# Kernel tuning notes

Hardware: AMD Instinct MI355X
Metric: run time of the kernel (lower is better)

Reference implementation:

```python
import jax, jax.numpy as jnp
import numpy as np

B, T, I, H = 64, 1024, 256, 256


def setup_inputs() -> dict:
    key = jax.random.key(0)
    ks = jax.random.split(key, 7)
    s_in = 1.0 / np.sqrt(I)
    s_h = 1.0 / np.sqrt(H)
    return {
        "x": jax.random.normal(ks[0], (B, T, I), dtype=jnp.float32),
        "W_ih0": jax.random.normal(ks[1], (H, I), dtype=jnp.float32) * s_in,
        "b_ih0": jax.random.normal(ks[2], (H,), dtype=jnp.float32) * s_in,
        "W_hh0": jax.random.normal(ks[3], (H, H), dtype=jnp.float32) * s_h,
        "W_ih1": jax.random.normal(ks[4], (H, H), dtype=jnp.float32) * s_h,
        "b_ih1": jax.random.normal(ks[5], (H,), dtype=jnp.float32) * s_h,
        "W_hh1": jax.random.normal(ks[6], (H, H), dtype=jnp.float32) * s_h,
    }


def _elman_layer(x, W_ih, b_ih, W_hh):
    # Batch the input projection across all timesteps (the fusion the torch
    # loop misses), then scan only the sequential hidden update.
    xp = jnp.einsum("bti,hi->bth", x, W_ih) + b_ih  # [B,T,H]
    h0 = jnp.zeros((x.shape[0], W_hh.shape[0]), dtype=x.dtype)

    def step(h, xt):  # xt: [B,H]
        h = jnp.tanh(xt + h @ W_hh.T)
        return h, h

    _, ys = jax.lax.scan(step, h0, jnp.swapaxes(xp, 0, 1))  # [T,B,H]
    return jnp.swapaxes(ys, 0, 1)  # [B,T,H]


def reference(x, W_ih0, b_ih0, W_hh0, W_ih1, b_ih1, W_hh1):
    h = _elman_layer(x, W_ih0, b_ih0, W_hh0)
    h = _elman_layer(h, W_ih1, b_ih1, W_hh1)
    return h
```

## Files before the change

### kernel.cpp

```cpp
#include <hip/hip_runtime.h>
#include <cstdint>


#define HDIM 256
#define TLEN 1024
#define BATCH 64

__global__ __launch_bounds__(256) void proj_gemm(
    const float* __restrict__ X,
    const float* __restrict__ W,
    const float* __restrict__ bias,
    float* __restrict__ C, int M)
{
    __shared__ __align__(16) float Ast[16][136];
    __shared__ __align__(16) float Bst[16][68];

    const int tid = threadIdx.x;
    const int tx  = tid & 15;
    const int ty  = tid >> 4;
    const int m0  = blockIdx.x * 128;
    const int n0  = blockIdx.y * 64;

    float acc[8][4];
#pragma unroll
    for (int i = 0; i < 8; ++i)
#pragma unroll
        for (int j = 0; j < 4; ++j) acc[i][j] = 0.f;

    const int ar = tid >> 1;
    const int ah = (tid & 1) * 8;
    const int bn = tid >> 2;
    const int bg = (tid & 3) * 4;

    for (int kc = 0; kc < 16; ++kc) {
        const int k0 = kc * 16;
        const float4 av0 = *reinterpret_cast<const float4*>(&X[(size_t)(m0 + ar) * HDIM + k0 + ah]);
        const float4 av1 = *reinterpret_cast<const float4*>(&X[(size_t)(m0 + ar) * HDIM + k0 + ah + 4]);
        const float4 bv  = *reinterpret_cast<const float4*>(&W[(size_t)(n0 + bn) * HDIM + k0 + bg]);
        __syncthreads();
        Ast[ah + 0][ar] = av0.x; Ast[ah + 1][ar] = av0.y;
        Ast[ah + 2][ar] = av0.z; Ast[ah + 3][ar] = av0.w;
        Ast[ah + 4][ar] = av1.x; Ast[ah + 5][ar] = av1.y;
        Ast[ah + 6][ar] = av1.z; Ast[ah + 7][ar] = av1.w;
        Bst[bg + 0][bn] = bv.x;  Bst[bg + 1][bn] = bv.y;
        Bst[bg + 2][bn] = bv.z;  Bst[bg + 3][bn] = bv.w;
        __syncthreads();
#pragma unroll
        for (int kk = 0; kk < 16; ++kk) {
            const float4 a0 = *reinterpret_cast<const float4*>(&Ast[kk][ty * 8]);
            const float4 a1 = *reinterpret_cast<const float4*>(&Ast[kk][ty * 8 + 4]);
            const float4 b4 = *reinterpret_cast<const float4*>(&Bst[kk][tx * 4]);
            const float av[8] = {a0.x, a0.y, a0.z, a0.w, a1.x, a1.y, a1.z, a1.w};
            const float bb[4] = {b4.x, b4.y, b4.z, b4.w};
#pragma unroll
            for (int i = 0; i < 8; ++i)
#pragma unroll
                for (int j = 0; j < 4; ++j)
                    acc[i][j] = fmaf(av[i], bb[j], acc[i][j]);
        }
    }

    const float4 bias4 = *reinterpret_cast<const float4*>(&bias[n0 + tx * 4]);
    const float bb[4] = {bias4.x, bias4.y, bias4.z, bias4.w};
#pragma unroll
    for (int i = 0; i < 8; ++i) {
        float4 o;
        o.x = acc[i][0] + bb[0];
        o.y = acc[i][1] + bb[1];
        o.z = acc[i][2] + bb[2];
        o.w = acc[i][3] + bb[3];
        *reinterpret_cast<float4*>(&C[(size_t)(m0 + ty * 8 + i) * HDIM + n0 + tx * 4]) = o;
    }
}

__device__ __forceinline__ float fast_tanh(float x)
{
    const float xc = fminf(fmaxf(x, -15.f), 15.f);
    const float e  = __expf(2.f * xc);
    return (e - 1.f) / (e + 1.f);
}

__global__ __launch_bounds__(1024) void elman_scan(
    const float* __restrict__ xp,
    const float* __restrict__ Whh,
    float* __restrict__ y,
    int T)
{
    const int b   = blockIdx.x;
    const int tid = threadIdx.x;
    const int j   = tid & 255;
    const int q   = tid >> 8;

    float4 w[16];
    const float4* wp = reinterpret_cast<const float4*>(Whh + (size_t)j * HDIM + q * 64);
#pragma unroll
    for (int c = 0; c < 16; ++c) w[c] = wp[c];

    __shared__ __align__(16) float hs[HDIM];
    __shared__ float red[3][HDIM];
    __shared__ float xpb[2][HDIM];

    const float* xrow = xp + (size_t)b * T * HDIM;
    float*       yrow = y  + (size_t)b * T * HDIM;

    if (q == 0) {
        hs[j] = 0.f;
        xpb[0][j] = xrow[j];
    }
    __syncthreads();

    for (int t = 0; t < T; ++t) {
        const float4* h4 = reinterpret_cast<const float4*>(&hs[q * 64]);
        float s0 = 0.f, s1 = 0.f, s2 = 0.f, s3 = 0.f;
#pragma unroll
        for (int c = 0; c < 16; c += 4) {
            const float4 h0 = h4[c + 0];
            const float4 h1 = h4[c + 1];
            const float4 h2 = h4[c + 2];
            const float4 h3 = h4[c + 3];
            s0 = fmaf(w[c + 0].x, h0.x, s0); s0 = fmaf(w[c + 0].y, h0.y, s0);
            s0 = fmaf(w[c + 0].z, h0.z, s0); s0 = fmaf(w[c + 0].w, h0.w, s0);
            s1 = fmaf(w[c + 1].x, h1.x, s1); s1 = fmaf(w[c + 1].y, h1.y, s1);
            s1 = fmaf(w[c + 1].z, h1.z, s1); s1 = fmaf(w[c + 1].w, h1.w, s1);
            s2 = fmaf(w[c + 2].x, h2.x, s2); s2 = fmaf(w[c + 2].y, h2.y, s2);
            s2 = fmaf(w[c + 2].z, h2.z, s2); s2 = fmaf(w[c + 2].w, h2.w, s2);
            s3 = fmaf(w[c + 3].x, h3.x, s3); s3 = fmaf(w[c + 3].y, h3.y, s3);
            s3 = fmaf(w[c + 3].z, h3.z, s3); s3 = fmaf(w[c + 3].w, h3.w, s3);
        }
        const float s = (s0 + s1) + (s2 + s3);

        if (q) red[q - 1][j] = s;
        __syncthreads();

        if (q == 0) {
            const float tot = s + red[0][j] + red[1][j] + red[2][j] + xpb[t & 1][j];
            const float hn  = fast_tanh(tot);
            hs[j] = hn;
            yrow[(size_t)t * HDIM + j] = hn;
        } else if (q == 1) {
            if (t + 1 < T) xpb[(t + 1) & 1][j] = xrow[(size_t)(t + 1) * HDIM + j];
        }
        __syncthreads();
    }
}

extern "C" void kernel_launch(void* const* d_in, const int* in_sizes, int n_in,
                              void* d_out, int out_size, void* d_ws, size_t ws_size,
                              hipStream_t stream)
{
    const float* x     = (const float*)d_in[0];
    const float* W_ih0 = (const float*)d_in[1];
    const float* b_ih0 = (const float*)d_in[2];
    const float* W_hh0 = (const float*)d_in[3];
    const float* W_ih1 = (const float*)d_in[4];
    const float* b_ih1 = (const float*)d_in[5];
    const float* W_hh1 = (const float*)d_in[6];

    float* out = (float*)d_out;
    float* xp  = (float*)d_ws;

    const int M = BATCH * TLEN;
    dim3 ggrid(M / 128, HDIM / 64);

    proj_gemm<<<ggrid, 256, 0, stream>>>(x,   W_ih0, b_ih0, xp, M);
    elman_scan<<<BATCH, 1024, 0, stream>>>(xp, W_hh0, out, TLEN);
    proj_gemm<<<ggrid, 256, 0, stream>>>(out, W_ih1, b_ih1, xp, M);
    elman_scan<<<BATCH, 1024, 0, stream>>>(xp, W_hh1, out, TLEN);
}
```

Measured before the change: 2.026 ms.

## Split recurrent dot across lane pairs with shuffle reduce and one barrier per step

The scan kernel drops from 1024 to 512 threads. Each hidden unit is now computed by two adjacent lanes, each holding half the W_hh row (128 floats) in registers, and the partial sums are combined with a shuffle instead of a shared-memory reduction. The hidden state is double-buffered in shared memory so each timestep needs one barrier instead of two, and the xp values are prefetched two steps ahead into registers. The cost is doubled register pressure per thread, which risks spills or lower occupancy, and a longer serial FMA chain per step.

```diff
diff --git a/kernel.cpp b/kernel.cpp
--- a/kernel.cpp
+++ b/kernel.cpp
@@ -80,67 +80,76 @@
     return (e - 1.f) / (e + 1.f);
 }
 
-__global__ __launch_bounds__(1024) void elman_scan(
+__device__ __forceinline__ float dot128(const float4* __restrict__ w,
+                                        const float*  __restrict__ hb)
+{
+    const float4* h4 = reinterpret_cast<const float4*>(hb);
+    float s0 = 0.f, s1 = 0.f, s2 = 0.f, s3 = 0.f;
+#pragma unroll
+    for (int c = 0; c < 32; c += 4) {
+        const float4 h0 = h4[c + 0];
+        const float4 h1 = h4[c + 1];
+        const float4 h2 = h4[c + 2];
+        const float4 h3 = h4[c + 3];
+        s0 = fmaf(w[c + 0].x, h0.x, s0); s0 = fmaf(w[c + 0].y, h0.y, s0);
+        s0 = fmaf(w[c + 0].z, h0.z, s0); s0 = fmaf(w[c + 0].w, h0.w, s0);
+        s1 = fmaf(w[c + 1].x, h1.x, s1); s1 = fmaf(w[c + 1].y, h1.y, s1);
+        s1 = fmaf(w[c + 1].z, h1.z, s1); s1 = fmaf(w[c + 1].w, h1.w, s1);
+        s2 = fmaf(w[c + 2].x, h2.x, s2); s2 = fmaf(w[c + 2].y, h2.y, s2);
+        s2 = fmaf(w[c + 2].z, h2.z, s2); s2 = fmaf(w[c + 2].w, h2.w, s2);
+        s3 = fmaf(w[c + 3].x, h3.x, s3); s3 = fmaf(w[c + 3].y, h3.y, s3);
+        s3 = fmaf(w[c + 3].z, h3.z, s3); s3 = fmaf(w[c + 3].w, h3.w, s3);
+    }
+    return (s0 + s1) + (s2 + s3);
+}
+
+__global__ __launch_bounds__(512, 2) void elman_scan(
     const float* __restrict__ xp,
     const float* __restrict__ Whh,
     float* __restrict__ y,
     int T)
 {
-    const int b   = blockIdx.x;
-    const int tid = threadIdx.x;
-    const int j   = tid & 255;
-    const int q   = tid >> 8;
+    const int b    = blockIdx.x;
+    const int tid  = threadIdx.x;
+    const int j    = tid >> 1;
+    const int half = tid & 1;
 
-    float4 w[16];
-    const float4* wp = reinterpret_cast<const float4*>(Whh + (size_t)j * HDIM + q * 64);
+    float4 w[32];
+    const float4* wp = reinterpret_cast<const float4*>(Whh + (size_t)j * HDIM + half * 128);
 #pragma unroll
-    for (int c = 0; c < 16; ++c) w[c] = wp[c];
+    for (int c = 0; c < 32; ++c) w[c] = wp[c];
 
-    __shared__ __align__(16) float hs[HDIM];
-    __shared__ float red[3][HDIM];
-    __shared__ float xpb[2][HDIM];
+    __shared__ __align__(16) float hbuf[2][HDIM];
 
     const float* xrow = xp + (size_t)b * T * HDIM;
     float*       yrow = y  + (size_t)b * T * HDIM;
 
-    if (q == 0) {
-        hs[j] = 0.f;
-        xpb[0][j] = xrow[j];
-    }
+    if (half == 0) hbuf[0][j] = 0.f;
+    float x0 = xrow[j];
+    float x1 = xrow[HDIM + j];
     __syncthreads();
 
-    for (int t = 0; t < T; ++t) {
-        const float4* h4 = reinterpret_cast<const float4*>(&hs[q * 64]);
-        float s0 = 0.f, s1 = 0.f, s2 = 0.f, s3 = 0.f;
-#pragma unroll
-        for (int c = 0; c < 16; c += 4) {
-            const float4 h0 = h4[c + 0];
-            const float4 h1 = h4[c + 1];
-            const float4 h2 = h4[c + 2];
-            const float4 h3 = h4[c + 3];
-            s0 = fmaf(w[c + 0].x, h0.x, s0); s0 = fmaf(w[c + 0].y, h0.y, s0);
-            s0 = fmaf(w[c + 0].z, h0.z, s0); s0 = fmaf(w[c + 0].w, h0.w, s0);
-            s1 = fmaf(w[c + 1].x, h1.x, s1); s1 = fmaf(w[c + 1].y, h1.y, s1);
-            s1 = fmaf(w[c + 1].z, h1.z, s1); s1 = fmaf(w[c + 1].w, h1.w, s1);
-            s2 = fmaf(w[c + 2].x, h2.x, s2); s2 = fmaf(w[c + 2].y, h2.y, s2);
-            s2 = fmaf(w[c + 2].z, h2.z, s2); s2 = fmaf(w[c + 2].w, h2.w, s2);
-            s3 = fmaf(w[c + 3].x, h3.x, s3); s3 = fmaf(w[c + 3].y, h3.y, s3);
-            s3 = fmaf(w[c + 3].z, h3.z, s3); s3 = fmaf(w[c + 3].w, h3.w, s3);
+    for (int t = 0; t < T; t += 2) {
+        {
+            const float xnew = (t + 2 < T) ? xrow[(size_t)(t + 2) * HDIM + j] : 0.f;
+            float s = dot128(w, &hbuf[0][half * 128]);
+            s += __shfl_xor(s, 1);
+            const float hn = fast_tanh(s + x0);
+            if (half == 0) hbuf[1][j] = hn;
+            else           yrow[(size_t)t * HDIM + j] = hn;
+            x0 = xnew;
+            __syncthreads();
         }
-        const float s = (s0 + s1) + (s2 + s3);
-
-        if (q) red[q - 1][j] = s;
-        __syncthreads();
-
-        if (q == 0) {
-            const float tot = s + red[0][j] + red[1][j] + red[2][j] + xpb[t & 1][j];
-            const float hn  = fast_tanh(tot);
-            hs[j] = hn;
-            yrow[(size_t)t * HDIM + j] = hn;
-        } else if (q == 1) {
-            if (t + 1 < T) xpb[(t + 1) & 1][j] = xrow[(size_t)(t + 1) * HDIM + j];
+        {
+            const float xnew = (t + 3 < T) ? xrow[(size_t)(t + 3) * HDIM + j] : 0.f;
+            float s = dot128(w, &hbuf[1][half * 128]);
+            s += __shfl_xor(s, 1);
+            const float hn = fast_tanh(s + x1);
+            if (half == 0) hbuf[0][j] = hn;
+            else           yrow[(size_t)(t + 1) * HDIM + j] = hn;
+            x1 = xnew;
+            __syncthreads();
         }
-        __syncthreads();
     }
 }
 
@@ -163,7 +172,7 @@
     dim3 ggrid(M / 128, HDIM / 64);
 
     proj_gemm<<<ggrid, 256, 0, stream>>>(x,   W_ih0, b_ih0, xp, M);
-    elman_scan<<<BATCH, 1024, 0, stream>>>(xp, W_hh0, out, TLEN);
+    elman_scan<<<BATCH, 512, 0, stream>>>(xp, W_hh0, out, TLEN);
     proj_gemm<<<ggrid, 256, 0, stream>>>(out, W_ih1, b_ih1, xp, M);
-    elman_scan<<<BATCH, 1024, 0, stream>>>(xp, W_hh1, out, TLEN);
+    elman_scan<<<BATCH, 512, 0, stream>>>(xp, W_hh1, out, TLEN);
 }
```

Result: slower. 2.460 ms (+21.4%).

## Reduce scan partial sums with wave shuffles and double-buffer hidden state

Applied to the files above, without the earlier changes.

The scan kernel now places the four K-quarter partial dot products for each hidden unit in adjacent lanes of one wave and combines them with xor shuffles, instead of going through a shared-memory reduction array. The hidden state is double-buffered in padded LDS, which cuts the per-timestep barriers from two to one. Input projections are prefetched into registers four steps ahead through a rolling buffer. The aim is to shorten the serial per-timestep critical path of barriers and LDS round-trips. In exchange, every lane now computes the tanh redundantly, and the launch_bounds occupancy hint may add register pressure.

```diff
diff --git a/kernel.cpp b/kernel.cpp
--- a/kernel.cpp
+++ b/kernel.cpp
@@ -5,6 +5,7 @@
 #define HDIM 256
 #define TLEN 1024
 #define BATCH 64
+#define HQ 68
 
 __global__ __launch_bounds__(256) void proj_gemm(
     const float* __restrict__ X,
@@ -80,67 +81,78 @@
     return (e - 1.f) / (e + 1.f);
 }
 
-__global__ __launch_bounds__(1024) void elman_scan(
+__global__ __launch_bounds__(1024, 4) void elman_scan(
     const float* __restrict__ xp,
     const float* __restrict__ Whh,
     float* __restrict__ y,
     int T)
 {
-    const int b   = blockIdx.x;
-    const int tid = threadIdx.x;
-    const int j   = tid & 255;
-    const int q   = tid >> 8;
+    const int b    = blockIdx.x;
+    const int tid  = threadIdx.x;
+    const int lane = tid & 63;
+    const int wave = tid >> 6;
+    const int j    = wave * 16 + (lane >> 2);
+    const int q    = lane & 3;
 
     float4 w[16];
-    const float4* wp = reinterpret_cast<const float4*>(Whh + (size_t)j * HDIM + q * 64);
+    {
+        const float4* wp = reinterpret_cast<const float4*>(Whh + (size_t)j * HDIM + q * 64);
 #pragma unroll
-    for (int c = 0; c < 16; ++c) w[c] = wp[c];
+        for (int c = 0; c < 16; ++c) w[c] = wp[c];
+    }
 
-    __shared__ __align__(16) float hs[HDIM];
-    __shared__ float red[3][HDIM];
-    __shared__ float xpb[2][HDIM];
+    __shared__ __align__(16) float hbuf[2][4 * HQ];
 
     const float* xrow = xp + (size_t)b * T * HDIM;
     float*       yrow = y  + (size_t)b * T * HDIM;
 
-    if (q == 0) {
-        hs[j] = 0.f;
-        xpb[0][j] = xrow[j];
-    }
+    const int hpos = (j >> 6) * HQ + (j & 63);
+    if (q == 0) hbuf[0][hpos] = 0.f;
+
+    float xv[4];
+#pragma unroll
+    for (int p = 0; p < 4; ++p) xv[p] = xrow[(size_t)p * HDIM + j];
+
     __syncthreads();
 
-    for (int t = 0; t < T; ++t) {
-        const float4* h4 = reinterpret_cast<const float4*>(&hs[q * 64]);
-        float s0 = 0.f, s1 = 0.f, s2 = 0.f, s3 = 0.f;
+    int cur = 0;
+    for (int t = 0; t < T; t += 4) {
 #pragma unroll
-        for (int c = 0; c < 16; c += 4) {
-            const float4 h0 = h4[c + 0];
-            const float4 h1 = h4[c + 1];
-            const float4 h2 = h4[c + 2];
-            const float4 h3 = h4[c + 3];
-            s0 = fmaf(w[c + 0].x, h0.x, s0); s0 = fmaf(w[c + 0].y, h0.y, s0);
-            s0 = fmaf(w[c + 0].z, h0.z, s0); s0 = fmaf(w[c + 0].w, h0.w, s0);
-            s1 = fmaf(w[c + 1].x, h1.x, s1); s1 = fmaf(w[c + 1].y, h1.y, s1);
-            s1 = fmaf(w[c + 1].z, h1.z, s1); s1 = fmaf(w[c + 1].w, h1.w, s1);
-            s2 = fmaf(w[c + 2].x, h2.x, s2); s2 = fmaf(w[c + 2].y, h2.y, s2);
-            s2 = fmaf(w[c + 2].z, h2.z, s2); s2 = fmaf(w[c + 2].w, h2.w, s2);
-            s3 = fmaf(w[c + 3].x, h3.x, s3); s3 = fmaf(w[c + 3].y, h3.y, s3);
-            s3 = fmaf(w[c + 3].z, h3.z, s3); s3 = fmaf(w[c + 3].w, h3.w, s3);
+        for (int p = 0; p < 4; ++p) {
+            int tf = t + p + 4; tf = (tf < T) ? tf : (T - 1);
+            const float xnew = xrow[(size_t)tf * HDIM + j];
+
+            const float* hb = &hbuf[cur][q * HQ];
+            float s0 = 0.f, s1 = 0.f, s2 = 0.f, s3 = 0.f;
+#pragma unroll
+            for (int c = 0; c < 16; c += 4) {
+                const float4 h0 = *reinterpret_cast<const float4*>(hb + (c + 0) * 4);
+                const float4 h1 = *reinterpret_cast<const float4*>(hb + (c + 1) * 4);
+                const float4 h2 = *reinterpret_cast<const float4*>(hb + (c + 2) * 4);
+                const float4 h3 = *reinterpret_cast<const float4*>(hb + (c + 3) * 4);
+                s0 = fmaf(w[c + 0].x, h0.x, s0); s0 = fmaf(w[c + 0].y, h0.y, s0);
+                s0 = fmaf(w[c + 0].z, h0.z, s0); s0 = fmaf(w[c + 0].w, h0.w, s0);
+                s1 = fmaf(w[c + 1].x, h1.x, s1); s1 = fmaf(w[c + 1].y, h1.y, s1);
+                s1 = fmaf(w[c + 1].z, h1.z, s1); s1 = fmaf(w[c + 1].w, h1.w, s1);
+                s2 = fmaf(w[c + 2].x, h2.x, s2); s2 = fmaf(w[c + 2].y, h2.y, s2);
+                s2 = fmaf(w[c + 2].z, h2.z, s2); s2 = fmaf(w[c + 2].w, h2.w, s2);
+                s3 = fmaf(w[c + 3].x, h3.x, s3); s3 = fmaf(w[c + 3].y, h3.y, s3);
+                s3 = fmaf(w[c + 3].z, h3.z, s3); s3 = fmaf(w[c + 3].w, h3.w, s3);
+            }
+            float s = (s0 + s1) + (s2 + s3);
+
+            s += __shfl_xor(s, 1);
+            s += __shfl_xor(s, 2);
+
+            const float hn = fast_tanh(s + xv[p]);
+
+            if (q == 0)      hbuf[cur ^ 1][hpos] = hn;
+            else if (q == 1) yrow[(size_t)(t + p) * HDIM + j] = hn;
+
+            xv[p] = xnew;
+            cur ^= 1;
+            __syncthreads();
         }
-        const float s = (s0 + s1) + (s2 + s3);
-
-        if (q) red[q - 1][j] = s;
-        __syncthreads();
-
-        if (q == 0) {
-            const float tot = s + red[0][j] + red[1][j] + red[2][j] + xpb[t & 1][j];
-            const float hn  = fast_tanh(tot);
-            hs[j] = hn;
-            yrow[(size_t)t * HDIM + j] = hn;
-        } else if (q == 1) {
-            if (t + 1 < T) xpb[(t + 1) & 1][j] = xrow[(size_t)(t + 1) * HDIM + j];
-        }
-        __syncthreads();
     }
 }
 
```

Result: faster. 1.773 ms (-12.5%).
